# Kernel tuning notes

Measured on AMD Instinct MI355X. Metric: run time of the kernel, lower is better.

## Reference

```python
import jax, jax.numpy as jnp
import numpy as np
import math

D_MODEL = 1024
N_HEAD = 16
D_HEAD = D_MODEL // N_HEAD


def setup_inputs() -> dict:
    key = jax.random.key(0)
    k0, k1, k2, k3, k4 = jax.random.split(key, 5)
    B, N = 4, 2048
    inp = jax.random.normal(k0, (B, N, D_MODEL), dtype=jnp.float32)
    # causal mask: True = keep (masked_fill on ~mask)
    mask = jnp.tril(jnp.ones((N, N), dtype=bool))
    # qkv_proj Linear(d_model, 3*d_model); output Linear(d_model, d_model)
    s_in = 1.0 / math.sqrt(D_MODEL)
    W_qkv = jax.random.uniform(k1, (D_MODEL, 3 * D_MODEL), jnp.float32, -s_in, s_in)
    b_qkv = jax.random.uniform(k2, (3 * D_MODEL,), jnp.float32, -s_in, s_in)
    W_out = jax.random.uniform(k3, (D_MODEL, D_MODEL), jnp.float32, -s_in, s_in)
    b_out = jax.random.uniform(k4, (D_MODEL,), jnp.float32, -s_in, s_in)
    return {"input": inp, "W_qkv": W_qkv, "b_qkv": b_qkv,
            "W_out": W_out, "b_out": b_out, "mask": mask}


def reference(input, W_qkv, b_qkv, W_out, b_out, mask):
    B, N, d = input.shape
    qkv = input @ W_qkv + b_qkv                       # [B,N,3d]  (dropout=eval no-op)
    q, k, v = jnp.split(qkv, 3, axis=-1)
    # [B,N,H,Dh] -> [B,H,N,Dh]
    q = q.reshape(B, N, N_HEAD, D_HEAD).transpose(0, 2, 1, 3)
    k = k.reshape(B, N, N_HEAD, D_HEAD).transpose(0, 2, 1, 3)
    v = v.reshape(B, N, N_HEAD, D_HEAD).transpose(0, 2, 1, 3)
    scale = 1.0 / math.sqrt(D_HEAD)
    scores = jnp.einsum('bhqd,bhkd->bhqk', q, k) * scale   # [B,H,N,N]
    scores = jnp.where(mask, scores, -jnp.inf)
    attn = jax.nn.softmax(scores, axis=-1)
    out = jnp.einsum('bhqk,bhkd->bhqd', attn, v)           # [B,H,N,Dh]
    out = out.transpose(0, 2, 1, 3).reshape(B, N, d)       # concat heads
    return out @ W_out + b_out
```

## Files before the change

kernel.cpp:

```cpp
#include <hip/hip_runtime.h>
#include <hip/hip_bf16.h>

typedef unsigned short u16;
typedef unsigned u32;
typedef __attribute__((ext_vector_type(4))) unsigned short u16x4;
typedef __attribute__((ext_vector_type(8))) unsigned short u16x8;
typedef __attribute__((ext_vector_type(4))) unsigned u32x4;
typedef __attribute__((ext_vector_type(8))) __bf16 bf16x8;
typedef __attribute__((ext_vector_type(4))) float f32x4;

typedef __attribute__((address_space(1))) void as1v;
typedef __attribute__((address_space(3))) void as3v;

#define MFMA16(a, b, c) __builtin_amdgcn_mfma_f32_16x16x32_bf16(a, b, c, 0, 0, 0)

__device__ __forceinline__ u16 f2bf(float f) {
    unsigned u = __builtin_bit_cast(unsigned, f);
    u += 0x7fffu + ((u >> 16) & 1u);
    return (u16)(u >> 16);
}

__device__ __forceinline__ u32 pkbf(float lo, float hi) {
    u32 r;
    asm("v_cvt_pk_bf16_f32 %0, %1, %2" : "=v"(r) : "v"(lo), "v"(hi));
    return r;
}

__device__ __forceinline__ void gload16(const void* g, void* l) {
    __builtin_amdgcn_global_load_lds((as1v*)g, (as3v*)l, 16, 0, 0);
}

__global__ void convert_f32_bf16(const float* __restrict__ in, u16* __restrict__ out, int n4) {
    int i = blockIdx.x * blockDim.x + threadIdx.x;
    if (i < n4) {
        float4 v = *(const float4*)&in[(size_t)i * 4];
        u16x4 o;
        o.x = f2bf(v.x); o.y = f2bf(v.y); o.z = f2bf(v.z); o.w = f2bf(v.w);
        *(u16x4*)&out[(size_t)i * 4] = o;
    }
}

__global__ void transpose_convert(const float* __restrict__ in, u16* __restrict__ out, int R, int C) {
    __shared__ float tl[64][65];
    const int rb = blockIdx.x, cb = blockIdx.y;
    const int tid = threadIdx.x;
    for (int it = 0; it < 4; ++it) {
        int lin = (tid + it * 256) * 4;
        int r = lin >> 6, c = lin & 63;
        float4 v = *(const float4*)&in[(size_t)(rb * 64 + r) * C + cb * 64 + c];
        tl[r][c + 0] = v.x; tl[r][c + 1] = v.y; tl[r][c + 2] = v.z; tl[r][c + 3] = v.w;
    }
    __syncthreads();
    for (int it = 0; it < 4; ++it) {
        int lin = (tid + it * 256) * 4;
        int oc = lin >> 6, orr = lin & 63;
        u16x4 o;
        o.x = f2bf(tl[orr + 0][oc]);
        o.y = f2bf(tl[orr + 1][oc]);
        o.z = f2bf(tl[orr + 2][oc]);
        o.w = f2bf(tl[orr + 3][oc]);
        *(u16x4*)&out[(size_t)(cb * 64 + oc) * R + rb * 64 + orr] = o;
    }
}

__global__ void transpose_v(const u16* __restrict__ vbuf, u16* __restrict__ vtb) {
    __shared__ u16 tl[64][65];
    const int nb = blockIdx.x, bh = blockIdx.y;
    const int tid = threadIdx.x;
    for (int it = 0; it < 2; ++it) {
        int lin = (tid + it * 256) * 8;
        int nl = lin >> 6, dh = lin & 63;
        u16x8 v = *(const u16x8*)&vbuf[((size_t)bh * 2048 + nb * 64 + nl) * 64 + dh];
#pragma unroll
        for (int j = 0; j < 8; ++j) tl[dh + j][nl] = v[j];
    }
    __syncthreads();
    for (int it = 0; it < 2; ++it) {
        int lin = (tid + it * 256) * 8;
        int dh = lin >> 6, nl = lin & 63;
        u16x8 o;
#pragma unroll
        for (int j = 0; j < 8; ++j) o[j] = tl[dh][nl + j];
        *(u16x8*)&vtb[((size_t)bh * 64 + dh) * 2048 + nb * 64 + nl] = o;
    }
}

__global__ __launch_bounds__(512, 2) void gemm256_qkv(
    const u16* __restrict__ A, const u16* __restrict__ Bt, const float* __restrict__ bias,
    u16* __restrict__ qb, u16* __restrict__ kb, u16* __restrict__ vb) {
    constexpr int K = 1024;
    constexpr int NT = 32;
    __shared__ u16 ldsu[65536];

    const int bid = blockIdx.x;
    const int swz = (bid & 7) * 48 + (bid >> 3);
    const int bm = swz / 12, bn = swz % 12;

    const int tid = threadIdx.x, wid = tid >> 6, lane = tid & 63;
    const int wr = wid >> 2, wc = wid & 3;
    const int l15 = lane & 15, lhi = lane >> 4;

    const int sslot = (lane & 7) ^ (lane >> 3);
    const int kcol = (sslot & 3) * 8;
    const int mloc = (lane >> 3) * 2 + (sslot >> 2);

    const u16* Arow[2];
    const u16* Brow[2];
#pragma unroll
    for (int li = 0; li < 2; ++li) {
        int sg = wid * 2 + li;
        int m = sg * 16 + mloc;
        Arow[li] = A + (size_t)(bm * 256 + m) * K + kcol;
        Brow[li] = Bt + (size_t)(bn * 256 + m) * K + kcol;
    }

    auto stageA = [&](int buf, int t) {
#pragma unroll
        for (int li = 0; li < 2; ++li) {
            int sg = wid * 2 + li;
            gload16(Arow[li] + t * 32, (char*)ldsu + buf * 32768 + sg * 1024);
        }
    };
    auto stageB = [&](int buf, int t) {
#pragma unroll
        for (int li = 0; li < 2; ++li) {
            int sg = wid * 2 + li;
            gload16(Brow[li] + t * 32, (char*)ldsu + buf * 32768 + 16384 + sg * 1024);
        }
    };

    const int rslot = ((l15 & 1) * 4 + lhi) ^ ((l15 >> 1) & 7);
    const int fragoff = (l15 >> 1) * 64 + rslot * 8;

    f32x4 acc[8][4];
#pragma unroll
    for (int i = 0; i < 8; ++i)
#pragma unroll
        for (int j = 0; j < 4; ++j) acc[i][j] = (f32x4){0.f, 0.f, 0.f, 0.f};

    auto doTile = [&](int cur, int tstage, bool dostage) {
        const u16* Ab = ldsu + cur * 16384 + wr * 4096 + fragoff;
        const u16* Bb = ldsu + cur * 16384 + 8192 + wc * 2048 + fragoff;
        bf16x8 af[8], b0, b1;
#pragma unroll
        for (int mf = 0; mf < 8; ++mf) af[mf] = *(const bf16x8*)(Ab + mf * 512);
        b0 = *(const bf16x8*)(Bb);
        b1 = *(const bf16x8*)(Bb + 512);
        if (dostage) stageA(tstage & 3, tstage);
        __builtin_amdgcn_s_setprio(1);
#pragma unroll
        for (int mf = 0; mf < 8; ++mf) {
            acc[mf][0] = MFMA16(af[mf], b0, acc[mf][0]);
            acc[mf][1] = MFMA16(af[mf], b1, acc[mf][1]);
        }
        __builtin_amdgcn_s_setprio(0);
        b0 = *(const bf16x8*)(Bb + 1024);
        b1 = *(const bf16x8*)(Bb + 1536);
        if (dostage) stageB(tstage & 3, tstage);
        __builtin_amdgcn_s_setprio(1);
#pragma unroll
        for (int mf = 0; mf < 8; ++mf) {
            acc[mf][2] = MFMA16(af[mf], b0, acc[mf][2]);
            acc[mf][3] = MFMA16(af[mf], b1, acc[mf][3]);
        }
        __builtin_amdgcn_s_setprio(0);
    };

    stageA(0, 0); stageB(0, 0);
    stageA(1, 1); stageB(1, 1);
    stageA(2, 2); stageB(2, 2);
    asm volatile("s_waitcnt vmcnt(8)" ::: "memory");
    __builtin_amdgcn_s_barrier();
    __builtin_amdgcn_sched_barrier(0);

    for (int t = 0; t < NT - 3; ++t) {
        doTile(t & 3, t + 3, true);
        asm volatile("s_waitcnt vmcnt(8)" ::: "memory");
        __builtin_amdgcn_s_barrier();
        __builtin_amdgcn_sched_barrier(0);
    }
    doTile((NT - 3) & 3, 0, false);
    asm volatile("s_waitcnt vmcnt(4)" ::: "memory");
    __builtin_amdgcn_s_barrier();
    __builtin_amdgcn_sched_barrier(0);
    doTile((NT - 2) & 3, 0, false);
    asm volatile("s_waitcnt vmcnt(0)" ::: "memory");
    __builtin_amdgcn_s_barrier();
    __builtin_amdgcn_sched_barrier(0);
    doTile((NT - 1) & 3, 0, false);

    const int bnbase = bn * 256 + wc * 64;
#pragma unroll
    for (int nf = 0; nf < 4; ++nf) {
        int cg = bnbase + nf * 16 + l15;
        float bv = bias[cg];
        int which = cg >> 10, rem = cg & 1023;
        u16* dst = (which == 0) ? qb : (which == 1) ? kb : vb;
        float qs = (which == 0) ? 0.18033688011112042f : 1.0f;
        size_t colterm = (size_t)(rem >> 6) * 131072 + (size_t)(rem & 63);
#pragma unroll
        for (int mf = 0; mf < 8; ++mf) {
            int rgb = bm * 256 + wr * 128 + mf * 16 + lhi * 4;
            size_t rowterm = (size_t)(rgb >> 11) * 2097152 + (size_t)(rgb & 2047) * 64;
#pragma unroll
            for (int v = 0; v < 4; ++v) {
                float val = (acc[mf][nf][v] + bv) * qs;
                dst[rowterm + (size_t)v * 64 + colterm] = f2bf(val);
            }
        }
    }
}

__global__ __launch_bounds__(256) void gemm_bt(
    const u16* __restrict__ A, const u16* __restrict__ Bt, const float* __restrict__ bias,
    int M, int N, int K, float* __restrict__ outf) {
    __shared__ u16 Al[128 * 32];
    __shared__ u16 Bl[128 * 32];
    const int bm = blockIdx.x, bn = blockIdx.y;
    const int tid = threadIdx.x, wid = tid >> 6, lane = tid & 63;
    const int wr = wid >> 1, wc = wid & 1;
    const int l15 = lane & 15, lhi = lane >> 4;

    f32x4 acc[4][4];
#pragma unroll
    for (int i = 0; i < 4; ++i)
#pragma unroll
        for (int j = 0; j < 4; ++j) acc[i][j] = (f32x4){0.f, 0.f, 0.f, 0.f};

    for (int k0 = 0; k0 < K; k0 += 32) {
        __syncthreads();
#pragma unroll
        for (int s = 0; s < 2; ++s) {
            int lin0 = (wid * 2 + s) * 1024;
            int off = lin0 + lane * 16;
            int row = off >> 6, colb = off & 63;
            const u16* ga = A + (size_t)(bm * 128 + row) * K + k0 + (colb >> 1);
            gload16(ga, (char*)Al + lin0);
            const u16* gb = Bt + (size_t)(bn * 128 + row) * K + k0 + (colb >> 1);
            gload16(gb, (char*)Bl + lin0);
        }
        __syncthreads();
        bf16x8 af[4], bfr[4];
#pragma unroll
        for (int mt = 0; mt < 4; ++mt)
            af[mt] = *(const bf16x8*)&Al[(wr * 64 + mt * 16 + l15) * 32 + lhi * 8];
#pragma unroll
        for (int nt = 0; nt < 4; ++nt)
            bfr[nt] = *(const bf16x8*)&Bl[(wc * 64 + nt * 16 + l15) * 32 + lhi * 8];
#pragma unroll
        for (int mt = 0; mt < 4; ++mt)
#pragma unroll
            for (int nt = 0; nt < 4; ++nt)
                acc[mt][nt] = MFMA16(af[mt], bfr[nt], acc[mt][nt]);
    }

#pragma unroll
    for (int mt = 0; mt < 4; ++mt)
#pragma unroll
        for (int nt = 0; nt < 4; ++nt)
#pragma unroll
            for (int v = 0; v < 4; ++v) {
                int rg = bm * 128 + wr * 64 + mt * 16 + lhi * 4 + v;
                int cg = bn * 128 + wc * 64 + nt * 16 + l15;
                outf[(size_t)rg * N + cg] = acc[mt][nt][v] + bias[cg];
            }
}

__global__ __launch_bounds__(256, 4) void attn_kernel(
    const u16* __restrict__ qbuf, const u16* __restrict__ kbuf,
    const u16* __restrict__ vtb, u16* __restrict__ obuf) {
    __shared__ u16 Kl[2][64 * 64];
    __shared__ u16 Vl[2][64 * 64];
    const int bid = blockIdx.x;
    const int idx = bid >> 3;
    const int c = 15 - (idx >> 3);
    const int bh = ((bid & 7) << 3) + (idx & 7);
    const int b = bh >> 4, h = bh & 15;
    const int tid = threadIdx.x, wid = tid >> 6, lane = tid & 63;
    const int l15 = lane & 15, lhi = lane >> 4;
    const int q0 = c * 128 + wid * 32;
    const int ntW = 2 * c + (wid >> 1) + 1;
    const int ntmax = 2 * c + 2;

    auto loadQ = [&](int qbase, bf16x8* dst) {
        const u16* qp = qbuf + ((size_t)bh * 2048 + qbase + l15) * 64 + lhi * 8;
        dst[0] = *(const bf16x8*)(qp);
        dst[1] = *(const bf16x8*)(qp + 32);
    };
    bf16x8 qf0[2], qf1[2];
    loadQ(q0, qf0); loadQ(q0 + 16, qf1);

    float m0 = -1e30f, l0 = 0.f, m1 = -1e30f, l1 = 0.f;
    f32x4 o0[4], o1[4];
#pragma unroll
    for (int d = 0; d < 4; ++d) {
        o0[d] = (f32x4){0.f, 0.f, 0.f, 0.f};
        o1[d] = (f32x4){0.f, 0.f, 0.f, 0.f};
    }

    const int srow = lane >> 3;
    const int scolb = ((lane & 7) * 16) ^ (srow << 4);

    auto stage = [&](int buf, int t) {
        const int kbase = t * 64;
#pragma unroll
        for (int s = 0; s < 2; ++s) {
            int sg = wid * 2 + s;
            int row = sg * 8 + srow;
            const u16* gk = kbuf + ((size_t)bh * 2048 + kbase + row) * 64 + (scolb >> 1);
            gload16(gk, (char*)Kl[buf] + sg * 1024);
            const u16* gv = vtb + ((size_t)bh * 64 + row) * 2048 + kbase + (scolb >> 1);
            gload16(gv, (char*)Vl[buf] + sg * 1024);
        }
    };

    auto smax = [&](f32x4* s, int qg0, int t, float& m, float& l, f32x4* oa, u32* pw) {
        const int qg = qg0 + l15;
        if (64 * t + 63 > qg0) {
#pragma unroll
            for (int kb4 = 0; kb4 < 4; ++kb4)
#pragma unroll
                for (int v = 0; v < 4; ++v) {
                    int kg = 64 * t + kb4 * 16 + lhi * 4 + v;
                    if (kg > qg) s[kb4][v] = -1e30f;
                }
        }
        float pm = fmaxf(fmaxf(fmaxf(s[0][0], s[0][1]), fmaxf(s[0][2], s[0][3])),
                         fmaxf(fmaxf(s[1][0], s[1][1]), fmaxf(s[1][2], s[1][3])));
        pm = fmaxf(pm, fmaxf(fmaxf(fmaxf(s[2][0], s[2][1]), fmaxf(s[2][2], s[2][3])),
                             fmaxf(fmaxf(s[3][0], s[3][1]), fmaxf(s[3][2], s[3][3]))));
        pm = fmaxf(pm, __shfl_xor(pm, 16, 64));
        pm = fmaxf(pm, __shfl_xor(pm, 32, 64));
        if (!__all(pm <= m + 8.f)) {
            float nm = fmaxf(m, pm);
            float f = exp2f(m - nm);
            m = nm;
            l *= f;
#pragma unroll
            for (int d = 0; d < 4; ++d)
#pragma unroll
                for (int v = 0; v < 4; ++v) oa[d][v] *= f;
        }
        float rs = 0.f;
#pragma unroll
        for (int kb4 = 0; kb4 < 4; ++kb4)
#pragma unroll
            for (int v = 0; v < 4; ++v) {
                float e = exp2f(s[kb4][v] - m);
                s[kb4][v] = e;
                rs += e;
            }
        rs += __shfl_xor(rs, 16, 64);
        rs += __shfl_xor(rs, 32, 64);
        l += rs;
        pw[0] = pkbf(s[0][0], s[0][1]); pw[1] = pkbf(s[0][2], s[0][3]);
        pw[2] = pkbf(s[1][0], s[1][1]); pw[3] = pkbf(s[1][2], s[1][3]);
        pw[4] = pkbf(s[2][0], s[2][1]); pw[5] = pkbf(s[2][2], s[2][3]);
        pw[6] = pkbf(s[3][0], s[3][1]); pw[7] = pkbf(s[3][2], s[3][3]);
    };

    auto computeChunk = [&](const char* Kb, const char* Vb, int t) {
        f32x4 s0[4], s1[4];
        __builtin_amdgcn_s_setprio(1);
#pragma unroll
        for (int kb4 = 0; kb4 < 4; ++kb4) {
            const int r = kb4 * 16 + l15;
            const int sw = (r & 7) << 4;
            const int rowb = r * 128;
            bf16x8 kf0 = *(const bf16x8*)(Kb + rowb + ((lhi * 16) ^ sw));
            bf16x8 kf1 = *(const bf16x8*)(Kb + rowb + ((64 + lhi * 16) ^ sw));
            f32x4 a0 = (f32x4){0.f, 0.f, 0.f, 0.f};
            a0 = MFMA16(kf0, qf0[0], a0);
            a0 = MFMA16(kf1, qf0[1], a0);
            s0[kb4] = a0;
            f32x4 a1 = (f32x4){0.f, 0.f, 0.f, 0.f};
            a1 = MFMA16(kf0, qf1[0], a1);
            a1 = MFMA16(kf1, qf1[1], a1);
            s1[kb4] = a1;
        }
        __builtin_amdgcn_s_setprio(0);
        u32 pw0[8], pw1[8];
        smax(s0, q0, t, m0, l0, o0, pw0);
        smax(s1, q0 + 16, t, m1, l1, o1, pw1);
        __builtin_amdgcn_s_setprio(1);
#pragma unroll
        for (int ks = 0; ks < 2; ++ks) {
            bf16x8 pb0 = __builtin_bit_cast(bf16x8,
                (u32x4){pw0[ks * 4 + 0], pw0[ks * 4 + 1], pw0[ks * 4 + 2], pw0[ks * 4 + 3]});
            bf16x8 pb1 = __builtin_bit_cast(bf16x8,
                (u32x4){pw1[ks * 4 + 0], pw1[ks * 4 + 1], pw1[ks * 4 + 2], pw1[ks * 4 + 3]});
#pragma unroll
            for (int dhb = 0; dhb < 4; ++dhb) {
                const int r = dhb * 16 + l15;
                const int sw = (r & 7) << 4;
                u16x4 v0 = *(const u16x4*)(Vb + r * 128 + ((ks * 64 + 8 * lhi) ^ sw));
                u16x4 v1 = *(const u16x4*)(Vb + r * 128 + ((ks * 64 + 32 + 8 * lhi) ^ sw));
                u16x8 vv = {v0[0], v0[1], v0[2], v0[3], v1[0], v1[1], v1[2], v1[3]};
                bf16x8 vf = __builtin_bit_cast(bf16x8, vv);
                o0[dhb] = MFMA16(vf, pb0, o0[dhb]);
                o1[dhb] = MFMA16(vf, pb1, o1[dhb]);
            }
        }
        __builtin_amdgcn_s_setprio(0);
    };

    stage(0, 0);
    int t = 0;
    for (;;) {
        __syncthreads();
        if (t + 1 < ntmax) stage(1, t + 1);
        if (t < ntW) computeChunk((const char*)Kl[0], (const char*)Vl[0], t);
        if (++t == ntmax) break;
        __syncthreads();
        if (t + 1 < ntmax) stage(0, t + 1);
        if (t < ntW) computeChunk((const char*)Kl[1], (const char*)Vl[1], t);
        if (++t == ntmax) break;
    }

    auto epi = [&](int qg0, float l, const f32x4* oa) {
        const float rl = 1.f / l;
        const int q = qg0 + l15;
        const size_t rowoff = ((size_t)b * 2048 + q) * 1024 + h * 64;
#pragma unroll
        for (int dhb = 0; dhb < 4; ++dhb) {
            u16x4 w;
#pragma unroll
            for (int v = 0; v < 4; ++v) w[v] = f2bf(oa[dhb][v] * rl);
            *(u16x4*)&obuf[rowoff + dhb * 16 + lhi * 4] = w;
        }
    };
    epi(q0, l0, o0);
    epi(q0 + 16, l1, o1);
}

extern "C" void kernel_launch(void* const* d_in, const int* in_sizes, int n_in,
                              void* d_out, int out_size, void* d_ws, size_t ws_size,
                              hipStream_t stream) {
    const float* inp   = (const float*)d_in[0];
    const float* W_qkv = (const float*)d_in[1];
    const float* b_qkv = (const float*)d_in[2];
    const float* W_out = (const float*)d_in[3];
    const float* b_out = (const float*)d_in[4];
    float* out = (float*)d_out;

    u16* xb   = (u16*)d_ws;
    u16* wqt  = xb + 8388608;
    u16* wot  = wqt + 3145728;
    u16* qbuf = wot + 1048576;
    u16* kbuf = qbuf + 8388608;
    u16* vbuf = kbuf + 8388608;
    u16* vtb  = vbuf + 8388608;
    u16* obuf = vtb + 8388608;

    convert_f32_bf16<<<8192, 256, 0, stream>>>(inp, xb, 2097152);
    transpose_convert<<<dim3(16, 48), 256, 0, stream>>>(W_qkv, wqt, 1024, 3072);
    transpose_convert<<<dim3(16, 16), 256, 0, stream>>>(W_out, wot, 1024, 1024);
    gemm256_qkv<<<384, 512, 0, stream>>>(xb, wqt, b_qkv, qbuf, kbuf, vbuf);
    transpose_v<<<dim3(32, 64), 256, 0, stream>>>(vbuf, vtb);
    attn_kernel<<<1024, 256, 0, stream>>>(qbuf, kbuf, vtb, obuf);
    gemm_bt<<<dim3(64, 8), 256, 0, stream>>>(obuf, wot, b_out, 8192, 1024, 1024, out);
}
```

Before: 192.0 us.

## Pipeline output GEMM, reorder attention blocks, use permlane swaps for reductions

Replaces the simple single-buffered output projection GEMM with a 256x128-tile, 512-thread kernel. It uses a 4-stage global_load_lds pipeline, swizzled LDS layout and block-index swizzling, interleaving loads with MFMA issue. The attention kernel's block-to-chunk mapping is changed to alternate heavy and light causal chunks. Its cross-lane softmax max/sum reductions use permlane16/32 swap builtins instead of shuffles when those builtins are available. The GEMM adds scheduling complexity and launches only 256 blocks.

```diff
diff --git a/kernel.cpp b/kernel.cpp
--- a/kernel.cpp
+++ b/kernel.cpp
@@ -14,6 +14,12 @@
 
 #define MFMA16(a, b, c) __builtin_amdgcn_mfma_f32_16x16x32_bf16(a, b, c, 0, 0, 0)
 
+#if __has_builtin(__builtin_amdgcn_permlane16_swap) && __has_builtin(__builtin_amdgcn_permlane32_swap)
+#define HAVE_PERMLANE_SWAP 1
+#else
+#define HAVE_PERMLANE_SWAP 0
+#endif
+
 __device__ __forceinline__ u16 f2bf(float f) {
     unsigned u = __builtin_bit_cast(unsigned, f);
     u += 0x7fffu + ((u >> 16) & 1u);
@@ -28,6 +34,38 @@
 
 __device__ __forceinline__ void gload16(const void* g, void* l) {
     __builtin_amdgcn_global_load_lds((as1v*)g, (as3v*)l, 16, 0, 0);
+}
+
+__device__ __forceinline__ float redmax_cross(float v) {
+#if HAVE_PERMLANE_SWAP
+    u32 xu = __builtin_bit_cast(u32, v);
+    auto r16 = __builtin_amdgcn_permlane16_swap(xu, xu, false, false);
+    float a = fmaxf(__builtin_bit_cast(float, (u32)r16[0]),
+                    __builtin_bit_cast(float, (u32)r16[1]));
+    u32 au = __builtin_bit_cast(u32, a);
+    auto r32 = __builtin_amdgcn_permlane32_swap(au, au, false, false);
+    return fmaxf(__builtin_bit_cast(float, (u32)r32[0]),
+                 __builtin_bit_cast(float, (u32)r32[1]));
+#else
+    v = fmaxf(v, __shfl_xor(v, 16, 64));
+    return fmaxf(v, __shfl_xor(v, 32, 64));
+#endif
+}
+
+__device__ __forceinline__ float redsum_cross(float v) {
+#if HAVE_PERMLANE_SWAP
+    u32 xu = __builtin_bit_cast(u32, v);
+    auto r16 = __builtin_amdgcn_permlane16_swap(xu, xu, false, false);
+    float a = __builtin_bit_cast(float, (u32)r16[0]) +
+              __builtin_bit_cast(float, (u32)r16[1]);
+    u32 au = __builtin_bit_cast(u32, a);
+    auto r32 = __builtin_amdgcn_permlane32_swap(au, au, false, false);
+    return __builtin_bit_cast(float, (u32)r32[0]) +
+           __builtin_bit_cast(float, (u32)r32[1]);
+#else
+    v += __shfl_xor(v, 16, 64);
+    return v + __shfl_xor(v, 32, 64);
+#endif
 }
 
 __global__ void convert_f32_bf16(const float* __restrict__ in, u16* __restrict__ out, int n4) {
@@ -211,59 +249,109 @@
     }
 }
 
-__global__ __launch_bounds__(256) void gemm_bt(
+__global__ __launch_bounds__(512, 2) void gemm256_out(
     const u16* __restrict__ A, const u16* __restrict__ Bt, const float* __restrict__ bias,
-    int M, int N, int K, float* __restrict__ outf) {
-    __shared__ u16 Al[128 * 32];
-    __shared__ u16 Bl[128 * 32];
-    const int bm = blockIdx.x, bn = blockIdx.y;
+    float* __restrict__ outf) {
+    constexpr int K = 1024;
+    constexpr int NT = 32;
+    __shared__ u16 ldsu[49152];
+
+    const int bid = blockIdx.x;
+    const int swz = (bid & 7) * 32 + (bid >> 3);
+    const int bm = swz >> 3, bn = swz & 7;
+
     const int tid = threadIdx.x, wid = tid >> 6, lane = tid & 63;
-    const int wr = wid >> 1, wc = wid & 1;
+    const int wr = wid >> 2, wc = wid & 3;
     const int l15 = lane & 15, lhi = lane >> 4;
 
-    f32x4 acc[4][4];
-#pragma unroll
-    for (int i = 0; i < 4; ++i)
-#pragma unroll
-        for (int j = 0; j < 4; ++j) acc[i][j] = (f32x4){0.f, 0.f, 0.f, 0.f};
-
-    for (int k0 = 0; k0 < K; k0 += 32) {
-        __syncthreads();
-#pragma unroll
-        for (int s = 0; s < 2; ++s) {
-            int lin0 = (wid * 2 + s) * 1024;
-            int off = lin0 + lane * 16;
-            int row = off >> 6, colb = off & 63;
-            const u16* ga = A + (size_t)(bm * 128 + row) * K + k0 + (colb >> 1);
-            gload16(ga, (char*)Al + lin0);
-            const u16* gb = Bt + (size_t)(bn * 128 + row) * K + k0 + (colb >> 1);
-            gload16(gb, (char*)Bl + lin0);
-        }
-        __syncthreads();
-        bf16x8 af[4], bfr[4];
-#pragma unroll
-        for (int mt = 0; mt < 4; ++mt)
-            af[mt] = *(const bf16x8*)&Al[(wr * 64 + mt * 16 + l15) * 32 + lhi * 8];
-#pragma unroll
-        for (int nt = 0; nt < 4; ++nt)
-            bfr[nt] = *(const bf16x8*)&Bl[(wc * 64 + nt * 16 + l15) * 32 + lhi * 8];
-#pragma unroll
-        for (int mt = 0; mt < 4; ++mt)
-#pragma unroll
-            for (int nt = 0; nt < 4; ++nt)
-                acc[mt][nt] = MFMA16(af[mt], bfr[nt], acc[mt][nt]);
-    }
-
-#pragma unroll
-    for (int mt = 0; mt < 4; ++mt)
-#pragma unroll
-        for (int nt = 0; nt < 4; ++nt)
-#pragma unroll
-            for (int v = 0; v < 4; ++v) {
-                int rg = bm * 128 + wr * 64 + mt * 16 + lhi * 4 + v;
-                int cg = bn * 128 + wc * 64 + nt * 16 + l15;
-                outf[(size_t)rg * N + cg] = acc[mt][nt][v] + bias[cg];
-            }
+    const int sslot = (lane & 7) ^ (lane >> 3);
+    const int kcol = (sslot & 3) * 8;
+    const int mloc = (lane >> 3) * 2 + (sslot >> 2);
+
+    const u16* Arow[2];
+#pragma unroll
+    for (int li = 0; li < 2; ++li) {
+        int sg = wid * 2 + li;
+        Arow[li] = A + (size_t)(bm * 256 + sg * 16 + mloc) * K + kcol;
+    }
+    const u16* Brow = Bt + (size_t)(bn * 128 + wid * 16 + mloc) * K + kcol;
+
+    auto stageA = [&](int buf, int t) {
+#pragma unroll
+        for (int li = 0; li < 2; ++li) {
+            int sg = wid * 2 + li;
+            gload16(Arow[li] + t * 32, (char*)ldsu + buf * 24576 + sg * 1024);
+        }
+    };
+    auto stageB = [&](int buf, int t) {
+        gload16(Brow + t * 32, (char*)ldsu + buf * 24576 + 16384 + wid * 1024);
+    };
+
+    const int rslot = ((l15 & 1) * 4 + lhi) ^ ((l15 >> 1) & 7);
+    const int fragoff = (l15 >> 1) * 64 + rslot * 8;
+
+    f32x4 acc[8][2];
+#pragma unroll
+    for (int i = 0; i < 8; ++i) {
+        acc[i][0] = (f32x4){0.f, 0.f, 0.f, 0.f};
+        acc[i][1] = (f32x4){0.f, 0.f, 0.f, 0.f};
+    }
+
+    auto doTile = [&](int cur, int tstage, bool dostage) {
+        const u16* Ab = ldsu + cur * 12288 + wr * 4096 + fragoff;
+        const u16* Bb = ldsu + cur * 12288 + 8192 + wc * 1024 + fragoff;
+        bf16x8 af[8], b0, b1;
+#pragma unroll
+        for (int mf = 0; mf < 8; ++mf) af[mf] = *(const bf16x8*)(Ab + mf * 512);
+        b0 = *(const bf16x8*)(Bb);
+        b1 = *(const bf16x8*)(Bb + 512);
+        if (dostage) stageA(tstage & 3, tstage);
+        __builtin_amdgcn_s_setprio(1);
+#pragma unroll
+        for (int mf = 0; mf < 8; ++mf) acc[mf][0] = MFMA16(af[mf], b0, acc[mf][0]);
+        __builtin_amdgcn_s_setprio(0);
+        if (dostage) stageB(tstage & 3, tstage);
+        __builtin_amdgcn_s_setprio(1);
+#pragma unroll
+        for (int mf = 0; mf < 8; ++mf) acc[mf][1] = MFMA16(af[mf], b1, acc[mf][1]);
+        __builtin_amdgcn_s_setprio(0);
+    };
+
+    stageA(0, 0); stageB(0, 0);
+    stageA(1, 1); stageB(1, 1);
+    stageA(2, 2); stageB(2, 2);
+    asm volatile("s_waitcnt vmcnt(6)" ::: "memory");
+    __builtin_amdgcn_s_barrier();
+    __builtin_amdgcn_sched_barrier(0);
+
+    for (int t = 0; t < NT - 3; ++t) {
+        doTile(t & 3, t + 3, true);
+        asm volatile("s_waitcnt vmcnt(6)" ::: "memory");
+        __builtin_amdgcn_s_barrier();
+        __builtin_amdgcn_sched_barrier(0);
+    }
+    doTile((NT - 3) & 3, 0, false);
+    asm volatile("s_waitcnt vmcnt(3)" ::: "memory");
+    __builtin_amdgcn_s_barrier();
+    __builtin_amdgcn_sched_barrier(0);
+    doTile((NT - 2) & 3, 0, false);
+    asm volatile("s_waitcnt vmcnt(0)" ::: "memory");
+    __builtin_amdgcn_s_barrier();
+    __builtin_amdgcn_sched_barrier(0);
+    doTile((NT - 1) & 3, 0, false);
+
+#pragma unroll
+    for (int nf = 0; nf < 2; ++nf) {
+        int cg = bn * 128 + wc * 32 + nf * 16 + l15;
+        float bv = bias[cg];
+#pragma unroll
+        for (int mf = 0; mf < 8; ++mf) {
+            int rgb = bm * 256 + wr * 128 + mf * 16 + lhi * 4;
+#pragma unroll
+            for (int v = 0; v < 4; ++v)
+                outf[(size_t)(rgb + v) * 1024 + cg] = acc[mf][nf][v] + bv;
+        }
+    }
 }
 
 __global__ __launch_bounds__(256, 4) void attn_kernel(
@@ -272,9 +360,11 @@
     __shared__ u16 Kl[2][64 * 64];
     __shared__ u16 Vl[2][64 * 64];
     const int bid = blockIdx.x;
-    const int idx = bid >> 3;
-    const int c = 15 - (idx >> 3);
-    const int bh = ((bid & 7) << 3) + (idx & 7);
+    const int rr = bid >> 8;
+    const int pp = (bid >> 6) & 3;
+    const int c = (rr & 1) ? (((rr >> 1) << 2) + pp)
+                           : (15 - ((rr >> 1) << 2) - pp);
+    const int bh = ((bid & 7) << 3) + ((bid >> 3) & 7);
     const int b = bh >> 4, h = bh & 15;
     const int tid = threadIdx.x, wid = tid >> 6, lane = tid & 63;
     const int l15 = lane & 15, lhi = lane >> 4;
@@ -329,8 +419,7 @@
                          fmaxf(fmaxf(s[1][0], s[1][1]), fmaxf(s[1][2], s[1][3])));
         pm = fmaxf(pm, fmaxf(fmaxf(fmaxf(s[2][0], s[2][1]), fmaxf(s[2][2], s[2][3])),
                              fmaxf(fmaxf(s[3][0], s[3][1]), fmaxf(s[3][2], s[3][3]))));
-        pm = fmaxf(pm, __shfl_xor(pm, 16, 64));
-        pm = fmaxf(pm, __shfl_xor(pm, 32, 64));
+        pm = redmax_cross(pm);
         if (!__all(pm <= m + 8.f)) {
             float nm = fmaxf(m, pm);
             float f = exp2f(m - nm);
@@ -350,9 +439,7 @@
                 s[kb4][v] = e;
                 rs += e;
             }
-        rs += __shfl_xor(rs, 16, 64);
-        rs += __shfl_xor(rs, 32, 64);
-        l += rs;
+        l += redsum_cross(rs);
         pw[0] = pkbf(s[0][0], s[0][1]); pw[1] = pkbf(s[0][2], s[0][3]);
         pw[2] = pkbf(s[1][0], s[1][1]); pw[3] = pkbf(s[1][2], s[1][3]);
         pw[4] = pkbf(s[2][0], s[2][1]); pw[5] = pkbf(s[2][2], s[2][3]);
@@ -458,5 +545,5 @@
     gemm256_qkv<<<384, 512, 0, stream>>>(xb, wqt, b_qkv, qbuf, kbuf, vbuf);
     transpose_v<<<dim3(32, 64), 256, 0, stream>>>(vbuf, vtb);
     attn_kernel<<<1024, 256, 0, stream>>>(qbuf, kbuf, vtb, obuf);
-    gemm_bt<<<dim3(64, 8), 256, 0, stream>>>(obuf, wot, b_out, 8192, 1024, 1024, out);
-}
+    gemm256_out<<<256, 512, 0, stream>>>(obuf, wot, b_out, out);
+}
```

Result: faster. 185.3 us (-3.4%).
